# Performance work log

Measured on AMD Instinct MI355X. Metric: run time of the kernel, lower is better.

## Reference

```python
import jax, jax.numpy as jnp
import numpy as np

N = 100000
E = 1600000
F_IN = 256
HEADS = 8
C1 = 8
NCLS = 16
NEG_SLOPE = 0.2


def setup_inputs() -> dict:
    key = jax.random.key(0)
    ks = jax.random.split(key, 8)
    x = jax.random.normal(ks[0], (N, F_IN), dtype=jnp.float32)
    edge_index = jax.random.randint(ks[1], (2, E), 0, N, dtype=jnp.int64)
    W1 = jax.random.normal(ks[2], (F_IN, HEADS * C1), dtype=jnp.float32) * (1.0 / np.sqrt(F_IN))
    a1_src = jax.random.normal(ks[3], (HEADS, C1), dtype=jnp.float32) * 0.1
    a1_dst = jax.random.normal(ks[4], (HEADS, C1), dtype=jnp.float32) * 0.1
    b1 = jnp.zeros((HEADS * C1,), dtype=jnp.float32)
    W2 = jax.random.normal(ks[5], (HEADS * C1, NCLS), dtype=jnp.float32) * (1.0 / np.sqrt(HEADS * C1))
    a2_src = jax.random.normal(ks[6], (1, NCLS), dtype=jnp.float32) * 0.1
    a2_dst = jax.random.normal(ks[7], (1, NCLS), dtype=jnp.float32) * 0.1
    b2 = jnp.zeros((NCLS,), dtype=jnp.float32)
    return {"x": x, "edge_index": edge_index, "W1": W1, "a1_src": a1_src,
            "a1_dst": a1_dst, "b1": b1, "W2": W2, "a2_src": a2_src,
            "a2_dst": a2_dst, "b2": b2}


def gat_layer(x, src, dst, W, a_src, a_dst, b, heads, out_c, concat):
    n = x.shape[0]
    h = (x @ W).reshape(n, heads, out_c)            # [N,H,C]
    al_src = (h * a_src).sum(-1)                    # [N,H]
    al_dst = (h * a_dst).sum(-1)                    # [N,H]
    e = jax.nn.leaky_relu(al_src[src] + al_dst[dst], NEG_SLOPE)  # [E',H]
    m = jax.ops.segment_max(e, dst, num_segments=n)              # per-dst max
    alpha = jnp.exp(e - m[dst])
    denom = jax.ops.segment_sum(alpha, dst, num_segments=n)
    alpha = alpha / denom[dst]
    out = jax.ops.segment_sum(h[src] * alpha[:, :, None], dst, num_segments=n)  # [N,H,C]
    out = out.reshape(n, heads * out_c) if concat else out.mean(axis=1)
    return out + b


def reference(x, edge_index, W1, a1_src, a1_dst, b1, W2, a2_src, a2_dst, b2):
    # add self-loops (PyG GATConv default)
    loop = jnp.arange(N, dtype=edge_index.dtype)
    src = jnp.concatenate([edge_index[0], loop])
    dst = jnp.concatenate([edge_index[1], loop])
    # dropout layers are identity in eval mode
    h = jax.nn.elu(gat_layer(x, src, dst, W1, a1_src, a1_dst, b1, HEADS, C1, True))
    out = gat_layer(h, src, dst, W2, a2_src, a2_dst, b2, 1, NCLS, False)
    return jax.nn.log_softmax(out, axis=-1)
```

## Files before the change

### kernel.cpp

```cpp
#include <hip/hip_runtime.h>
#include <math.h>

#define NN   100000
#define EE   1600000
#define FIN  256
#define NCLS 16
#define NEG  0.2f

#define NEDGE (EE + NN)
#define WBKT  256
#define NBKT  ((NN + WBKT - 1) / WBKT)
#define CAP   5120
#define ABLK  4096
#define NABLK ((NEDGE + ABLK - 1) / ABLK)

#define OFF_GCNT  0
#define OFF_BASE  392
#define OFF_ROW   784
#define OFF_BKT   100788
#define OFF_ADJ   (OFF_BKT + NBKT*CAP)
#define OFF_H1B   (OFF_ADJ + NEDGE)
#define OFF_H1E   (OFF_H1B + NN*32)
#define OFF_AL1S  (OFF_H1E + NN*32)
#define OFF_AL1D  (OFF_AL1S + NN*8)
#define OFF_H2B   (OFF_AL1D + NN*8)
#define OFF_AL2S  (OFF_H2B + NN*8)
#define OFF_AL2D  (OFF_AL2S + NN)

__device__ __forceinline__ float lrelu(float x) { return x >= 0.f ? x : NEG * x; }
__device__ __forceinline__ unsigned short f2bf(float x) {
    unsigned u = __float_as_uint(x);
    return (unsigned short)((u + 0x7FFF + ((u >> 16) & 1)) >> 16);
}
__device__ __forceinline__ float bf2f(unsigned short b) {
    return __uint_as_float(((unsigned)b) << 16);
}
__device__ __forceinline__ float bflo(unsigned u) { return __uint_as_float(u << 16); }
__device__ __forceinline__ float bfhi(unsigned u) { return __uint_as_float(u & 0xFFFF0000u); }

__global__ __launch_bounds__(256) void k_binA(
    const int* __restrict__ esrc, const int* __restrict__ edst,
    int* __restrict__ gcnt, unsigned* __restrict__ bkt)
{
    __shared__ int lcnt[NBKT];
    __shared__ int lbase[NBKT];
    const int t = threadIdx.x;
    const int e0 = blockIdx.x * ABLK;
    for (int i = t; i < NBKT; i += 256) lcnt[i] = 0;
    __syncthreads();

    unsigned wrd[16];
    unsigned short bb[16], ll[16];
    #pragma unroll
    for (int j = 0; j < 16; ++j) {
        int ei = e0 + j * 256 + t;
        bb[j] = 0xFFFFu;
        if (ei < NEDGE) {
            int s, d;
            if (ei < EE) { s = esrc[ei]; d = edst[ei]; } else { s = d = ei - EE; }
            int b = d >> 8;
            wrd[j] = ((unsigned)s << 8) | (unsigned)(d & 255);
            bb[j] = (unsigned short)b;
            ll[j] = (unsigned short)atomicAdd(&lcnt[b], 1);
        }
    }
    __syncthreads();
    for (int i = t; i < NBKT; i += 256)
        lbase[i] = lcnt[i] ? atomicAdd(&gcnt[i], lcnt[i]) : 0;
    __syncthreads();
    #pragma unroll
    for (int j = 0; j < 16; ++j) {
        if (bb[j] != 0xFFFFu) {
            int b = bb[j];
            bkt[(size_t)b * CAP + lbase[b] + ll[j]] = wrd[j];
        }
    }
}

__global__ __launch_bounds__(512) void k_scanB(
    const int* __restrict__ gcnt, int* __restrict__ base, int* __restrict__ row)
{
    __shared__ int s[512];
    int t = threadIdx.x;
    int v = (t < NBKT) ? gcnt[t] : 0;
    s[t] = v;
    __syncthreads();
    for (int off = 1; off < 512; off <<= 1) {
        int u = (t >= off) ? s[t - off] : 0;
        __syncthreads();
        s[t] += u;
        __syncthreads();
    }
    if (t <= NBKT) base[t] = s[t] - v;
    if (t == 0) row[NN] = NEDGE;
}

__global__ __launch_bounds__(256) void k_binC(
    const int* __restrict__ gcnt, const int* __restrict__ base,
    const unsigned* __restrict__ bkt, int* __restrict__ row, int* __restrict__ adj)
{
    __shared__ unsigned wd[CAP];
    __shared__ int hist[256], pref[256], cnt2[256];
    const int g = blockIdx.x, t = threadIdx.x;
    const int cn = gcnt[g], bs = base[g];
    hist[t] = 0; cnt2[t] = 0;
    __syncthreads();
    for (int i = t; i < cn; i += 256) {
        unsigned w = bkt[(size_t)g * CAP + i];
        wd[i] = w;
        atomicAdd(&hist[w & 255], 1);
    }
    __syncthreads();
    int v = hist[t];
    pref[t] = v;
    __syncthreads();
    for (int off = 1; off < 256; off <<= 1) {
        int u = (t >= off) ? pref[t - off] : 0;
        __syncthreads();
        pref[t] += u;
        __syncthreads();
    }
    int ex = pref[t] - v;
    int n = g * 256 + t;
    if (n < NN) row[n] = bs + ex;
    pref[t] = ex;
    __syncthreads();
    for (int i = t; i < cn; i += 256) {
        unsigned w = wd[i];
        int dl = w & 255;
        int p = atomicAdd(&cnt2[dl], 1);
        adj[bs + pref[dl] + p] = (int)(w >> 8);
    }
}

__global__ __launch_bounds__(256) void k_gemm1(
    const float* __restrict__ x, const float* __restrict__ W1,
    const float* __restrict__ a1s, const float* __restrict__ a1d,
    unsigned short* __restrict__ h1b, float* __restrict__ al1s, float* __restrict__ al1d)
{
    __shared__ float sxT[32][68];
    __shared__ float sW[32][64];
    const int t = threadIdx.x;
    const int n0 = blockIdx.x * 64;
    const int tr = t >> 4, tc = t & 15;

    float acc[4][4] = {};

    for (int kc = 0; kc < 256; kc += 32) {
        __syncthreads();
        #pragma unroll
        for (int it = 0; it < 2; ++it) {
            int i = t + it * 256;
            int r = i >> 3, fj = i & 7;
            int n = n0 + r;
            float4 v = (n < NN) ? *(const float4*)(x + (size_t)n * FIN + kc + fj * 4)
                                : make_float4(0.f, 0.f, 0.f, 0.f);
            sxT[fj * 4 + 0][r] = v.x;
            sxT[fj * 4 + 1][r] = v.y;
            sxT[fj * 4 + 2][r] = v.z;
            sxT[fj * 4 + 3][r] = v.w;
        }
        #pragma unroll
        for (int it = 0; it < 2; ++it) {
            int i = t + it * 256;
            int r = i >> 4, fj = i & 15;
            *(float4*)&sW[r][fj * 4] = *(const float4*)(W1 + (size_t)(kc + r) * 64 + fj * 4);
        }
        __syncthreads();
        #pragma unroll
        for (int k = 0; k < 32; ++k) {
            float4 a = *(const float4*)&sxT[k][tr * 4];
            float4 b = *(const float4*)&sW[k][tc * 4];
            acc[0][0] += a.x * b.x; acc[0][1] += a.x * b.y; acc[0][2] += a.x * b.z; acc[0][3] += a.x * b.w;
            acc[1][0] += a.y * b.x; acc[1][1] += a.y * b.y; acc[1][2] += a.y * b.z; acc[1][3] += a.y * b.w;
            acc[2][0] += a.z * b.x; acc[2][1] += a.z * b.y; acc[2][2] += a.z * b.z; acc[2][3] += a.z * b.w;
            acc[3][0] += a.w * b.x; acc[3][1] += a.w * b.y; acc[3][2] += a.w * b.z; acc[3][3] += a.w * b.w;
        }
    }

    #pragma unroll
    for (int j = 0; j < 4; ++j) {
        int n = n0 + tr * 4 + j;
        if (n < NN) {
            ushort4 v = make_ushort4(f2bf(acc[j][0]), f2bf(acc[j][1]), f2bf(acc[j][2]), f2bf(acc[j][3]));
            *(ushort4*)(h1b + (size_t)n * 64 + tc * 4) = v;
        }
    }

    float sa[4], da[4];
    #pragma unroll
    for (int u = 0; u < 4; ++u) { sa[u] = a1s[tc * 4 + u]; da[u] = a1d[tc * 4 + u]; }
    #pragma unroll
    for (int j = 0; j < 4; ++j) {
        float vs = acc[j][0] * sa[0] + acc[j][1] * sa[1] + acc[j][2] * sa[2] + acc[j][3] * sa[3];
        float vd = acc[j][0] * da[0] + acc[j][1] * da[1] + acc[j][2] * da[2] + acc[j][3] * da[3];
        vs += __shfl_xor(vs, 1, 64);
        vd += __shfl_xor(vd, 1, 64);
        int n = n0 + tr * 4 + j;
        if (!(tc & 1) && n < NN) {
            al1s[n * 8 + (tc >> 1)] = vs;
            al1d[n * 8 + (tc >> 1)] = vd;
        }
    }
}

__global__ __launch_bounds__(256) void k_agg1(
    const int* __restrict__ row, const int* __restrict__ adj,
    const float* __restrict__ al1s, const float* __restrict__ al1d,
    const unsigned* __restrict__ h1b2, const float* __restrict__ b1,
    unsigned* __restrict__ h1e2)
{
    const int wv = threadIdx.x >> 6, lane = threadIdx.x & 63;
    const int n = blockIdx.x * 4 + wv;
    const int half = lane >> 5;
    const int cp   = lane & 31;
    const int h    = cp >> 2;
    const float ald = al1d[n * 8 + h];
    const int r0 = row[n], r1 = row[n + 1];

    float dsum = 0.f, ax = 0.f, ay = 0.f;
    int i = r0;
    for (; i + 3 < r1; i += 4) {
        int i0 = i + half, i1 = i + 2 + half;
        int s0 = adj[i0], s1 = adj[i1];
        float w0 = __expf(lrelu(al1s[s0 * 8 + h] + ald));
        float w1 = __expf(lrelu(al1s[s1 * 8 + h] + ald));
        unsigned u0 = h1b2[s0 * 32 + cp];
        unsigned u1 = h1b2[s1 * 32 + cp];
        dsum += w0 + w1;
        ax += w0 * bflo(u0) + w1 * bflo(u1);
        ay += w0 * bfhi(u0) + w1 * bfhi(u1);
    }
    for (; i < r1; i += 2) {
        int i0 = i + half;
        bool act = i0 < r1;
        int s0 = adj[act ? i0 : r0];
        float w0 = act ? __expf(lrelu(al1s[s0 * 8 + h] + ald)) : 0.f;
        unsigned u0 = h1b2[s0 * 32 + cp];
        dsum += w0;
        ax += w0 * bflo(u0);
        ay += w0 * bfhi(u0);
    }
    dsum += __shfl_xor(dsum, 32, 64);
    ax   += __shfl_xor(ax, 32, 64);
    ay   += __shfl_xor(ay, 32, 64);

    float inv = 1.f / dsum;
    float vx = ax * inv + b1[cp * 2];
    float vy = ay * inv + b1[cp * 2 + 1];
    vx = vx > 0.f ? vx : __expf(vx) - 1.f;
    vy = vy > 0.f ? vy : __expf(vy) - 1.f;
    if (half == 0)
        h1e2[n * 32 + cp] = (unsigned)f2bf(vx) | ((unsigned)f2bf(vy) << 16);
}

__global__ __launch_bounds__(256) void k_gemm2(
    const unsigned short* __restrict__ h1e, const float* __restrict__ W2,
    const float* __restrict__ a2s, const float* __restrict__ a2d,
    unsigned short* __restrict__ h2b, float* __restrict__ al2s, float* __restrict__ al2d)
{
    __shared__ float sW[64 * 16];
    const int t = threadIdx.x;
    for (int i = t; i < 64 * 16; i += 256) sW[i] = W2[i];
    __syncthreads();
    const int n = blockIdx.x * 16 + (t >> 4);
    const int k = t & 15;
    if (n >= NN) return;
    const unsigned short* hr = h1e + (size_t)n * 64;
    float acc = 0.f;
    #pragma unroll
    for (int c = 0; c < 64; ++c) acc += bf2f(hr[c]) * sW[c * 16 + k];
    h2b[(size_t)n * 16 + k] = f2bf(acc);
    float vs = acc * a2s[k], vd = acc * a2d[k];
    #pragma unroll
    for (int off = 1; off < 16; off <<= 1) {
        vs += __shfl_xor(vs, off, 64);
        vd += __shfl_xor(vd, off, 64);
    }
    if (k == 0) { al2s[n] = vs; al2d[n] = vd; }
}

__global__ __launch_bounds__(256) void k_agg2(
    const int* __restrict__ row, const int* __restrict__ adj,
    const float* __restrict__ al2s, const float* __restrict__ al2d,
    const unsigned* __restrict__ h2b2, const float* __restrict__ b2,
    float* __restrict__ out)
{
    const int wv = threadIdx.x >> 6, lane = threadIdx.x & 63;
    const int n = blockIdx.x * 4 + wv;
    const float ald = al2d[n];
    const int r0 = row[n], r1 = row[n + 1];

    const int j = lane >> 3;
    const int c = lane & 7;
    float dsum = 0.f, ax = 0.f, ay = 0.f;
    for (int i = r0; i < r1; i += 8) {
        int i0 = i + j;
        bool act = i0 < r1;
        int s = adj[act ? i0 : r0];
        float w = act ? __expf(lrelu(al2s[s] + ald)) : 0.f;
        unsigned u = h2b2[s * 8 + c];
        dsum += w;
        ax += w * bflo(u);
        ay += w * bfhi(u);
    }
    #pragma unroll
    for (int off = 8; off < 64; off <<= 1) {
        dsum += __shfl_xor(dsum, off, 64);
        ax   += __shfl_xor(ax, off, 64);
        ay   += __shfl_xor(ay, off, 64);
    }
    float inv = 1.f / dsum;
    float vx = ax * inv + b2[c * 2];
    float vy = ay * inv + b2[c * 2 + 1];

    float mx = fmaxf(vx, vy);
    #pragma unroll
    for (int off = 1; off < 8; off <<= 1) mx = fmaxf(mx, __shfl_xor(mx, off, 64));
    float se = __expf(vx - mx) + __expf(vy - mx);
    #pragma unroll
    for (int off = 1; off < 8; off <<= 1) se += __shfl_xor(se, off, 64);
    float ls = mx + __logf(se);
    if (j == 0)
        *(float2*)(out + (size_t)n * 16 + c * 2) = make_float2(vx - ls, vy - ls);
}

extern "C" void kernel_launch(void* const* d_in, const int* in_sizes, int n_in,
                              void* d_out, int out_size, void* d_ws, size_t ws_size,
                              hipStream_t stream)
{
    const float* x    = (const float*)d_in[0];
    const int*   eidx = (const int*)d_in[1];
    const float* W1   = (const float*)d_in[2];
    const float* a1s  = (const float*)d_in[3];
    const float* a1d  = (const float*)d_in[4];
    const float* b1   = (const float*)d_in[5];
    const float* W2   = (const float*)d_in[6];
    const float* a2s  = (const float*)d_in[7];
    const float* a2d  = (const float*)d_in[8];
    const float* b2   = (const float*)d_in[9];
    float* out = (float*)d_out;
    float* ws  = (float*)d_ws;

    const int* esrc = eidx;
    const int* edst = eidx + EE;

    int* gcnt = (int*)(ws + OFF_GCNT);
    int* base = (int*)(ws + OFF_BASE);
    int* row  = (int*)(ws + OFF_ROW);
    unsigned* bkt = (unsigned*)(ws + OFF_BKT);
    int* adj  = (int*)(ws + OFF_ADJ);
    unsigned short* h1b = (unsigned short*)(ws + OFF_H1B);
    unsigned short* h1e = (unsigned short*)(ws + OFF_H1E);
    float* al1s  = ws + OFF_AL1S;
    float* al1d  = ws + OFF_AL1D;
    unsigned short* h2b = (unsigned short*)(ws + OFF_H2B);
    float* al2s  = ws + OFF_AL2S;
    float* al2d  = ws + OFF_AL2D;

    hipMemsetAsync(gcnt, 0, 392 * sizeof(int), stream);

    k_binA <<<NABLK, 256, 0, stream>>>(esrc, edst, gcnt, bkt);
    k_scanB<<<1,     512, 0, stream>>>(gcnt, base, row);
    k_binC <<<NBKT,  256, 0, stream>>>(gcnt, base, bkt, row, adj);

    k_gemm1<<<(NN + 63) / 64, 256, 0, stream>>>(x, W1, a1s, a1d, h1b, al1s, al1d);
    k_agg1 <<<NN / 4, 256, 0, stream>>>(row, adj, al1s, al1d, (const unsigned*)h1b, b1, (unsigned*)h1e);
    k_gemm2<<<NN / 16, 256, 0, stream>>>(h1e, W2, a2s, a2d, h2b, al2s, al2d);
    k_agg2 <<<NN / 4, 256, 0, stream>>>(row, adj, al2s, al2d, (const unsigned*)h2b, b2, out);
}
```

Measured before the change: 390.0 us.

## Vectorize agg1 gathers to 16-byte loads per head, add nontemporal hints

The layer-1 aggregation kernel is reorganised so each lane handles one head for one of eight concurrent edges and gathers a full 16-byte bf16 row segment, instead of pairs of lanes splitting edges with 4-byte loads. The goal is fewer, wider gather transactions and more edges in flight per wave, with the reduction done by cross-lane shuffles. The gemm2 input is read with 16-byte vector loads, bucket writes and reads and the adjacency reads use nontemporal hints, and agg2's bounds-check select is removed. In exchange the kernels hold more accumulator registers and use more shuffles. gemm2's n<NN guard is dropped, which is only safe because NN divides evenly.

```diff
diff --git a/kernel.cpp b/kernel.cpp
--- a/kernel.cpp
+++ b/kernel.cpp
@@ -27,6 +27,8 @@
 #define OFF_AL2S  (OFF_H2B + NN*8)
 #define OFF_AL2D  (OFF_AL2S + NN)
 
+typedef unsigned uv4 __attribute__((ext_vector_type(4)));
+
 __device__ __forceinline__ float lrelu(float x) { return x >= 0.f ? x : NEG * x; }
 __device__ __forceinline__ unsigned short f2bf(float x) {
     unsigned u = __float_as_uint(x);
@@ -72,7 +74,7 @@
     for (int j = 0; j < 16; ++j) {
         if (bb[j] != 0xFFFFu) {
             int b = bb[j];
-            bkt[(size_t)b * CAP + lbase[b] + ll[j]] = wrd[j];
+            __builtin_nontemporal_store(wrd[j], &bkt[(size_t)b * CAP + lbase[b] + ll[j]]);
         }
     }
 }
@@ -106,7 +108,7 @@
     hist[t] = 0; cnt2[t] = 0;
     __syncthreads();
     for (int i = t; i < cn; i += 256) {
-        unsigned w = bkt[(size_t)g * CAP + i];
+        unsigned w = __builtin_nontemporal_load(&bkt[(size_t)g * CAP + i]);
         wd[i] = w;
         atomicAdd(&hist[w & 255], 1);
     }
@@ -207,55 +209,65 @@
 __global__ __launch_bounds__(256) void k_agg1(
     const int* __restrict__ row, const int* __restrict__ adj,
     const float* __restrict__ al1s, const float* __restrict__ al1d,
-    const unsigned* __restrict__ h1b2, const float* __restrict__ b1,
-    unsigned* __restrict__ h1e2)
+    const uv4* __restrict__ h1bq, const float* __restrict__ b1,
+    uv4* __restrict__ h1eq)
 {
     const int wv = threadIdx.x >> 6, lane = threadIdx.x & 63;
     const int n = blockIdx.x * 4 + wv;
-    const int half = lane >> 5;
-    const int cp   = lane & 31;
-    const int h    = cp >> 2;
+    const int eg = lane >> 3;
+    const int h  = lane & 7;
     const float ald = al1d[n * 8 + h];
     const int r0 = row[n], r1 = row[n + 1];
 
-    float dsum = 0.f, ax = 0.f, ay = 0.f;
-    int i = r0;
-    for (; i + 3 < r1; i += 4) {
-        int i0 = i + half, i1 = i + 2 + half;
-        int s0 = adj[i0], s1 = adj[i1];
-        float w0 = __expf(lrelu(al1s[s0 * 8 + h] + ald));
-        float w1 = __expf(lrelu(al1s[s1 * 8 + h] + ald));
-        unsigned u0 = h1b2[s0 * 32 + cp];
-        unsigned u1 = h1b2[s1 * 32 + cp];
-        dsum += w0 + w1;
-        ax += w0 * bflo(u0) + w1 * bflo(u1);
-        ay += w0 * bfhi(u0) + w1 * bfhi(u1);
-    }
-    for (; i < r1; i += 2) {
-        int i0 = i + half;
-        bool act = i0 < r1;
-        int s0 = adj[act ? i0 : r0];
-        float w0 = act ? __expf(lrelu(al1s[s0 * 8 + h] + ald)) : 0.f;
-        unsigned u0 = h1b2[s0 * 32 + cp];
-        dsum += w0;
-        ax += w0 * bflo(u0);
-        ay += w0 * bfhi(u0);
-    }
-    dsum += __shfl_xor(dsum, 32, 64);
-    ax   += __shfl_xor(ax, 32, 64);
-    ay   += __shfl_xor(ay, 32, 64);
+    float dsum = 0.f;
+    float a0 = 0.f, a1 = 0.f, a2 = 0.f, a3 = 0.f;
+    float a4 = 0.f, a5 = 0.f, a6 = 0.f, a7 = 0.f;
+    #pragma unroll 2
+    for (int i = r0 + eg; i < r1; i += 8) {
+        int s = __builtin_nontemporal_load(&adj[i]);
+        float w = __expf(lrelu(al1s[s * 8 + h] + ald));
+        uv4 u = __builtin_nontemporal_load(&h1bq[s * 8 + h]);
+        dsum += w;
+        a0 += w * bflo(u.x); a1 += w * bfhi(u.x);
+        a2 += w * bflo(u.y); a3 += w * bfhi(u.y);
+        a4 += w * bflo(u.z); a5 += w * bfhi(u.z);
+        a6 += w * bflo(u.w); a7 += w * bfhi(u.w);
+    }
+    #pragma unroll
+    for (int off = 8; off < 64; off <<= 1) {
+        dsum += __shfl_xor(dsum, off, 64);
+        a0 += __shfl_xor(a0, off, 64); a1 += __shfl_xor(a1, off, 64);
+        a2 += __shfl_xor(a2, off, 64); a3 += __shfl_xor(a3, off, 64);
+        a4 += __shfl_xor(a4, off, 64); a5 += __shfl_xor(a5, off, 64);
+        a6 += __shfl_xor(a6, off, 64); a7 += __shfl_xor(a7, off, 64);
+    }
+    if (eg != 0) return;
 
     float inv = 1.f / dsum;
-    float vx = ax * inv + b1[cp * 2];
-    float vy = ay * inv + b1[cp * 2 + 1];
-    vx = vx > 0.f ? vx : __expf(vx) - 1.f;
-    vy = vy > 0.f ? vy : __expf(vy) - 1.f;
-    if (half == 0)
-        h1e2[n * 32 + cp] = (unsigned)f2bf(vx) | ((unsigned)f2bf(vy) << 16);
+    float4 bL = *(const float4*)(b1 + h * 8);
+    float4 bH = *(const float4*)(b1 + h * 8 + 4);
+    float v0 = a0 * inv + bL.x, v1 = a1 * inv + bL.y;
+    float v2 = a2 * inv + bL.z, v3 = a3 * inv + bL.w;
+    float v4 = a4 * inv + bH.x, v5 = a5 * inv + bH.y;
+    float v6 = a6 * inv + bH.z, v7 = a7 * inv + bH.w;
+    v0 = v0 > 0.f ? v0 : __expf(v0) - 1.f;
+    v1 = v1 > 0.f ? v1 : __expf(v1) - 1.f;
+    v2 = v2 > 0.f ? v2 : __expf(v2) - 1.f;
+    v3 = v3 > 0.f ? v3 : __expf(v3) - 1.f;
+    v4 = v4 > 0.f ? v4 : __expf(v4) - 1.f;
+    v5 = v5 > 0.f ? v5 : __expf(v5) - 1.f;
+    v6 = v6 > 0.f ? v6 : __expf(v6) - 1.f;
+    v7 = v7 > 0.f ? v7 : __expf(v7) - 1.f;
+    uv4 o;
+    o.x = (unsigned)f2bf(v0) | ((unsigned)f2bf(v1) << 16);
+    o.y = (unsigned)f2bf(v2) | ((unsigned)f2bf(v3) << 16);
+    o.z = (unsigned)f2bf(v4) | ((unsigned)f2bf(v5) << 16);
+    o.w = (unsigned)f2bf(v6) | ((unsigned)f2bf(v7) << 16);
+    h1eq[n * 8 + h] = o;
 }
 
 __global__ __launch_bounds__(256) void k_gemm2(
-    const unsigned short* __restrict__ h1e, const float* __restrict__ W2,
+    const uv4* __restrict__ h1eq, const float* __restrict__ W2,
     const float* __restrict__ a2s, const float* __restrict__ a2d,
     unsigned short* __restrict__ h2b, float* __restrict__ al2s, float* __restrict__ al2d)
 {
@@ -265,11 +277,16 @@
     __syncthreads();
     const int n = blockIdx.x * 16 + (t >> 4);
     const int k = t & 15;
-    if (n >= NN) return;
-    const unsigned short* hr = h1e + (size_t)n * 64;
+    const uv4* hr = h1eq + (size_t)n * 8;
     float acc = 0.f;
     #pragma unroll
-    for (int c = 0; c < 64; ++c) acc += bf2f(hr[c]) * sW[c * 16 + k];
+    for (int q = 0; q < 8; ++q) {
+        uv4 u = hr[q];
+        acc += bflo(u.x) * sW[(q * 8 + 0) * 16 + k] + bfhi(u.x) * sW[(q * 8 + 1) * 16 + k]
+             + bflo(u.y) * sW[(q * 8 + 2) * 16 + k] + bfhi(u.y) * sW[(q * 8 + 3) * 16 + k]
+             + bflo(u.z) * sW[(q * 8 + 4) * 16 + k] + bfhi(u.z) * sW[(q * 8 + 5) * 16 + k]
+             + bflo(u.w) * sW[(q * 8 + 6) * 16 + k] + bfhi(u.w) * sW[(q * 8 + 7) * 16 + k];
+    }
     h2b[(size_t)n * 16 + k] = f2bf(acc);
     float vs = acc * a2s[k], vd = acc * a2d[k];
     #pragma unroll
@@ -294,11 +311,10 @@
     const int j = lane >> 3;
     const int c = lane & 7;
     float dsum = 0.f, ax = 0.f, ay = 0.f;
-    for (int i = r0; i < r1; i += 8) {
-        int i0 = i + j;
-        bool act = i0 < r1;
-        int s = adj[act ? i0 : r0];
-        float w = act ? __expf(lrelu(al2s[s] + ald)) : 0.f;
+    #pragma unroll 2
+    for (int i = r0 + j; i < r1; i += 8) {
+        int s = __builtin_nontemporal_load(&adj[i]);
+        float w = __expf(lrelu(al2s[s] + ald));
         unsigned u = h2b2[s * 8 + c];
         dsum += w;
         ax += w * bflo(u);
@@ -351,7 +367,8 @@
     unsigned* bkt = (unsigned*)(ws + OFF_BKT);
     int* adj  = (int*)(ws + OFF_ADJ);
     unsigned short* h1b = (unsigned short*)(ws + OFF_H1B);
-    unsigned short* h1e = (unsigned short*)(ws + OFF_H1E);
+    uv4* h1bq = (uv4*)(ws + OFF_H1B);
+    uv4* h1eq = (uv4*)(ws + OFF_H1E);
     float* al1s  = ws + OFF_AL1S;
     float* al1d  = ws + OFF_AL1D;
     unsigned short* h2b = (unsigned short*)(ws + OFF_H2B);
@@ -365,7 +382,7 @@
     k_binC <<<NBKT,  256, 0, stream>>>(gcnt, base, bkt, row, adj);
 
     k_gemm1<<<(NN + 63) / 64, 256, 0, stream>>>(x, W1, a1s, a1d, h1b, al1s, al1d);
-    k_agg1 <<<NN / 4, 256, 0, stream>>>(row, adj, al1s, al1d, (const unsigned*)h1b, b1, (unsigned*)h1e);
-    k_gemm2<<<NN / 16, 256, 0, stream>>>(h1e, W2, a2s, a2d, h2b, al2s, al2d);
+    k_agg1 <<<NN / 4, 256, 0, stream>>>(row, adj, al1s, al1d, h1bq, b1, h1eq);
+    k_gemm2<<<NN / 16, 256, 0, stream>>>(h1eq, W2, a2s, a2d, h2b, al2s, al2d);
     k_agg2 <<<NN / 4, 256, 0, stream>>>(row, adj, al2s, al2d, (const unsigned*)h2b, b2, out);
 }
```

Measured after the change: 432.1 us. 10.8% more time.
